# Kernel optimization log

Measured on AMD Instinct MI355X. Metric: run time of the kernel, lower is better.

## Reference

```python
import jax, jax.numpy as jnp
import numpy as np

V, BLK, L, H, C, FF = 50257, 2048, 6, 8, 512, 2048
D = C // H  # head_dim = 64

def setup_inputs() -> dict:
    key = jax.random.key(0)
    ks = jax.random.split(key, 16)
    s = 0.02
    proj_std = 0.02 / np.sqrt(2 * L)
    return {
        'idx': jax.random.randint(ks[0], (2, 2048), 0, V, dtype=jnp.int64),
        'wte': jax.random.normal(ks[1], (V, C), jnp.float32) * s,
        'wpe': jax.random.normal(ks[2], (BLK, C), jnp.float32) * s,
        'ln1_w': jnp.ones((L, C), jnp.float32), 'ln1_b': jnp.zeros((L, C), jnp.float32),
        'c_attn_w': jax.random.normal(ks[3], (L, 3 * C, C), jnp.float32) * s,
        'c_proj_w': jax.random.normal(ks[4], (L, C, C), jnp.float32) * proj_std,
        'ln2_w': jnp.ones((L, C), jnp.float32), 'ln2_b': jnp.zeros((L, C), jnp.float32),
        'fc_w': jax.random.normal(ks[5], (L, FF, C), jnp.float32) * s,
        'proj_w': jax.random.normal(ks[6], (L, C, FF), jnp.float32) * proj_std,
        'lnf_w': jnp.ones((C,), jnp.float32), 'lnf_b': jnp.zeros((C,), jnp.float32),
    }

def _layernorm(x, w, b, eps=1e-5):
    mu = jnp.mean(x, axis=-1, keepdims=True)
    var = jnp.var(x, axis=-1, keepdims=True)
    return (x - mu) * jax.lax.rsqrt(var + eps) * w + b

def _attn(x, attn_w, proj_w, mask):
    B, T, _ = x.shape
    qkv = jnp.einsum('btc,fc->btf', x, attn_w)  # (B,T,3C)
    q, k, v = jnp.split(qkv, 3, axis=-1)
    q = q.reshape(B, T, H, D)
    k = k.reshape(B, T, H, D)
    v = v.reshape(B, T, H, D)
    scale = 1.0 / np.sqrt(D)
    att = jnp.einsum('bthd,bshd->bhts', q, k) * scale  # (B,H,T,T)
    att = jnp.where(mask, att, -jnp.inf)
    att = jax.nn.softmax(att, axis=-1)
    y = jnp.einsum('bhts,bshd->bthd', att, v).reshape(B, T, C)
    return jnp.einsum('btc,oc->bto', y, proj_w)

def reference(idx, wte, wpe, ln1_w, ln1_b, c_attn_w, c_proj_w, ln2_w, ln2_b, fc_w, proj_w, lnf_w, lnf_b):
    B, T = idx.shape
    pos = jnp.arange(T)
    x = wte[idx] + wpe[pos]  # (B,T,C); dropout p=0
    mask = jnp.tril(jnp.ones((T, T), bool))[None, None]
    for i in range(L):
        x = x + _attn(_layernorm(x, ln1_w[i], ln1_b[i]), c_attn_w[i], c_proj_w[i], mask)
        h = _layernorm(x, ln2_w[i], ln2_b[i])
        h = jax.nn.gelu(jnp.einsum('btc,fc->btf', h, fc_w[i]), approximate=False)
        x = x + jnp.einsum('btf,cf->btc', h, proj_w[i])
    x = _layernorm(x, lnf_w, lnf_b)
    logits = jnp.einsum('btc,vc->btv', x, wte)  # tied lm_head
    return logits
```

## Files before the change

kernel.cpp:

```cpp
#include <hip/hip_runtime.h>

typedef unsigned short u16;
typedef short bf16x8 __attribute__((ext_vector_type(8)));
typedef float f32x4 __attribute__((ext_vector_type(4)));
typedef unsigned short u16x4 __attribute__((ext_vector_type(4)));
typedef unsigned short u16x8 __attribute__((ext_vector_type(8)));
typedef unsigned int u32x2 __attribute__((ext_vector_type(2)));

#define B_ 2
#define T_ 2048
#define C_ 512
#define H_ 8
#define FF_ 2048
#define L_ 6
#define V_ 50257
#define M_ (B_*T_)

__device__ __forceinline__ u16 f2b(float f) {
  union { float f; unsigned u; } v; v.f = f;
  unsigned r = v.u + 0x7FFFu + ((v.u >> 16) & 1u);
  return (u16)(r >> 16);
}
__device__ __forceinline__ float b2f(u16 u) {
  union { unsigned u; float f; } v; v.u = ((unsigned)u) << 16; return v.f;
}
__device__ __forceinline__ unsigned pk_bf16(float lo, float hi) {
  unsigned r;
  asm volatile("v_cvt_pk_bf16_f32 %0, %1, %2" : "=v"(r) : "v"(lo), "v"(hi));
  return r;
}
__device__ __forceinline__ float exp2_fast(float x) {
  float r; asm("v_exp_f32 %0, %1" : "=v"(r) : "v"(x)); return r;
}
__device__ __forceinline__ float rcp_fast(float x) {
  float r; asm("v_rcp_f32 %0, %1" : "=v"(r) : "v"(x)); return r;
}

__device__ __forceinline__ void async16(const void* g, void* l) {
  __builtin_amdgcn_global_load_lds((const __attribute__((address_space(1))) unsigned int*)g,
                                   (__attribute__((address_space(3))) unsigned int*)l, 16, 0, 0);
}

template<int N> __device__ __forceinline__ void vwait() {
  if constexpr (N == 0) asm volatile("s_waitcnt vmcnt(0)" ::: "memory");
  else if constexpr (N == 2) asm volatile("s_waitcnt vmcnt(2)" ::: "memory");
  else if constexpr (N == 3) asm volatile("s_waitcnt vmcnt(3)" ::: "memory");
  else if constexpr (N == 4) asm volatile("s_waitcnt vmcnt(4)" ::: "memory");
}

__device__ __forceinline__ bf16x8 scale8(u16x8 v, float s) {
  union { bf16x8 b; unsigned u[4]; } r;
#pragma unroll
  for (int i = 0; i < 4; i++)
    r.u[i] = pk_bf16(b2f(v[2*i]) * s, b2f(v[2*i+1]) * s);
  return r.b;
}

struct CvtArgs { const f32x4* s[5]; u16x4* d[5]; };
__global__ void cvt_all_k(CvtArgs a) {
  const int sizes[5] = { V_*C_/4, L_*3*C_*C_/4, L_*C_*C_/4, L_*FF_*C_/4, L_*C_*FF_/4 };
  int gid = blockIdx.x * blockDim.x + threadIdx.x;
  int stride = gridDim.x * blockDim.x;
#pragma unroll
  for (int seg = 0; seg < 5; seg++) {
    const f32x4* src = a.s[seg];
    u16x4* dst = a.d[seg];
    for (int i = gid; i < sizes[seg]; i += stride) {
      f32x4 v = src[i];
      u16x4 o;
      o[0] = f2b(v[0]); o[1] = f2b(v[1]); o[2] = f2b(v[2]); o[3] = f2b(v[3]);
      dst[i] = o;
    }
  }
}

__global__ void embed_k(const int* __restrict__ idx, const float* __restrict__ wte,
                        const float* __restrict__ wpe, float* __restrict__ x) {
  int t = blockIdx.x * 256 + threadIdx.x;
  int row = t >> 7;
  int c4 = t & 127;
  int tok = idx[row];
  int pos = row & (T_ - 1);
  f32x4 a = ((const f32x4*)(wte + (long)tok * C_))[c4];
  f32x4 p = ((const f32x4*)(wpe + (long)pos * C_))[c4];
  ((f32x4*)x)[t] = a + p;
}

__global__ void ln_k(const float* __restrict__ x, const float* __restrict__ w,
                     const float* __restrict__ b, u16* __restrict__ out) {
  int wv = threadIdx.x >> 6;
  int lane = threadIdx.x & 63;
  int row = blockIdx.x * 4 + wv;
  const f32x4* xr = (const f32x4*)(x + (long)row * C_);
  f32x4 v0 = xr[lane * 2], v1 = xr[lane * 2 + 1];
  float s = 0.f, s2 = 0.f;
#pragma unroll
  for (int j = 0; j < 4; j++) { s += v0[j] + v1[j]; s2 += v0[j]*v0[j] + v1[j]*v1[j]; }
#pragma unroll
  for (int off = 32; off >= 1; off >>= 1) { s += __shfl_xor(s, off); s2 += __shfl_xor(s2, off); }
  float mu = s * (1.f / C_);
  float inv = rsqrtf(s2 * (1.f / C_) - mu * mu + 1e-5f);
  const f32x4* wr = (const f32x4*)w;
  const f32x4* br = (const f32x4*)b;
  f32x4 w0 = wr[lane*2], w1 = wr[lane*2+1], b0 = br[lane*2], b1 = br[lane*2+1];
  u16x8 o;
#pragma unroll
  for (int j = 0; j < 4; j++) {
    o[j]     = f2b((v0[j] - mu) * inv * w0[j] + b0[j]);
    o[j + 4] = f2b((v1[j] - mu) * inv * w1[j] + b1[j]);
  }
  *(u16x8*)(out + (long)row * C_ + lane * 8) = o;
}

template<int EPI, int BM, int BN>
__global__ __launch_bounds__(256) void gemm_bt_k(
    const u16* __restrict__ A, const u16* __restrict__ Bw,
    u16* __restrict__ Cb, float* __restrict__ Cf,
    int N, int K, int ldc)
{
  constexpr int MT = BM / 32;
  constexpr int NT = BN / 32;
  constexpr int AJ = BM / 64;
  constexpr int BJ = BN / 64;
  constexpr int LPT = AJ + BJ;
  __shared__ __align__(16) u16 sA[3][BM * 32];
  __shared__ __align__(16) u16 sB[3][BN * 32];
  const int tid = threadIdx.x;
  const int n0 = blockIdx.x * BN;
  const int m0 = blockIdx.y * BM;
  const int w = tid >> 6;
  const int lane = tid & 63;
  const int wm = (w >> 1) * (BM / 2);
  const int wn = (w & 1) * (BN / 2);
  const int g = lane >> 4;
  const int l15 = lane & 15;
  const int sw3 = l15 & 3;

  f32x4 acc[MT][NT] = {};

  const int nk = K >> 5;
  const int ksw = ((tid & 3) ^ ((tid >> 2) & 3)) * 8;
  const u16* gA[AJ];
  const u16* gB[BJ];
#pragma unroll
  for (int j = 0; j < AJ; j++)
    gA[j] = A + (long)(m0 + (tid >> 2) + j * 64) * K + ksw;
#pragma unroll
  for (int j = 0; j < BJ; j++)
    gB[j] = Bw + (long)(n0 + (tid >> 2) + j * 64) * K + ksw;

  auto stage = [&](int buf, int kt) {
    int ko = kt << 5;
#pragma unroll
    for (int j = 0; j < AJ; j++)
      async16(gA[j] + ko, &sA[buf][(j * 256 + w * 64) * 8]);
#pragma unroll
    for (int j = 0; j < BJ; j++)
      async16(gB[j] + ko, &sB[buf][(j * 256 + w * 64) * 8]);
  };

  stage(0, 0);
  stage(1, 1);
  int cur = 0, nxt = 2;
  for (int kt = 0; kt < nk; kt++) {
    if (kt + 1 < nk) vwait<LPT>(); else vwait<0>();
    __builtin_amdgcn_s_barrier();
    if (kt + 2 < nk) stage(nxt, kt + 2);
    const u16* pa = sA[cur];
    const u16* pb = sB[cur];
    bf16x8 af[MT], bfr[NT];
#pragma unroll
    for (int mt = 0; mt < MT; mt++)
      af[mt] = *(const bf16x8*)(pa + (wm + mt * 16 + l15) * 32 + ((g ^ sw3) * 8));
#pragma unroll
    for (int nt = 0; nt < NT; nt++)
      bfr[nt] = *(const bf16x8*)(pb + (wn + nt * 16 + l15) * 32 + ((g ^ sw3) * 8));
#pragma unroll
    for (int mt = 0; mt < MT; mt++)
#pragma unroll
      for (int nt = 0; nt < NT; nt++)
        acc[mt][nt] = __builtin_amdgcn_mfma_f32_16x16x32_bf16(af[mt], bfr[nt], acc[mt][nt], 0, 0, 0);
    cur = (cur == 2) ? 0 : cur + 1;
    nxt = (nxt == 2) ? 0 : nxt + 1;
  }

#pragma unroll
  for (int mt = 0; mt < MT; mt++) {
    int m = m0 + wm + mt * 16 + g * 4;
#pragma unroll
    for (int nt = 0; nt < NT; nt++) {
      int n = n0 + wn + nt * 16 + l15;
      f32x4 v = acc[mt][nt];
#pragma unroll
      for (int r = 0; r < 4; r++) {
        long ci = (long)(m + r) * ldc + n;
        if (EPI == 0) {
          Cb[ci] = f2b(v[r]);
        } else if (EPI == 1) {
          Cf[ci] += v[r];
        } else {
          float f = v[r];
          float u = f * f;
          float inner = f * (0.7978845608028654f + 0.03567740814183056f * u);
          inner = fminf(fmaxf(inner, -15.f), 15.f);
          float a = exp2_fast(2.8853900817779268f * inner);
          Cb[ci] = f2b(f * a * rcp_fast(a + 1.0f));
        }
      }
    }
  }
}

__global__ __launch_bounds__(512) void gemm_lmhead_k(
    const u16* __restrict__ A, const u16* __restrict__ Bw,
    float* __restrict__ Cf, int N)
{
  __shared__ __align__(16) u16 sA[3][256 * 32];
  __shared__ __align__(16) u16 sB[3][128 * 32];
  const int K = 512;
  const int bid = blockIdx.x;
  const int swz = (bid & 7) * 786 + (bid >> 3);
  const int n0 = (swz % 393) * 128;
  const int m0 = (swz / 393) * 256;
  const int tid = threadIdx.x;
  const int w = tid >> 6;
  const int lane = tid & 63;
  const int wm = (w >> 1) * 64;
  const int wn = (w & 1) * 64;
  const int g = lane >> 4;
  const int l15 = lane & 15;
  const int sw3 = l15 & 3;

  f32x4 acc[4][4] = {};

  const int ksw = ((tid & 3) ^ ((tid >> 2) & 3)) * 8;
  const u16* gA[2];
#pragma unroll
  for (int j = 0; j < 2; j++)
    gA[j] = A + (long)(m0 + (tid >> 2) + j * 128) * K + ksw;
  int brow = n0 + (tid >> 2); if (brow > N - 1) brow = N - 1;
  const u16* gB0 = Bw + (long)brow * K + ksw;

  auto stage = [&](int buf, int kt) {
    int ko = kt << 5;
#pragma unroll
    for (int j = 0; j < 2; j++)
      async16(gA[j] + ko, &sA[buf][(j * 512 + w * 64) * 8]);
    async16(gB0 + ko, &sB[buf][(w * 64) * 8]);
  };

  stage(0, 0);
  stage(1, 1);
  int cur = 0, nxt = 2;
  const int nk = K >> 5;
  for (int kt = 0; kt < nk; kt++) {
    if (kt + 1 < nk) vwait<3>(); else vwait<0>();
    __builtin_amdgcn_s_barrier();
    if (kt + 2 < nk) stage(nxt, kt + 2);
    const u16* pa = sA[cur];
    const u16* pb = sB[cur];
    bf16x8 af[4], bfr[4];
#pragma unroll
    for (int mt = 0; mt < 4; mt++)
      af[mt] = *(const bf16x8*)(pa + (wm + mt * 16 + l15) * 32 + ((g ^ sw3) * 8));
#pragma unroll
    for (int nt = 0; nt < 4; nt++)
      bfr[nt] = *(const bf16x8*)(pb + (wn + nt * 16 + l15) * 32 + ((g ^ sw3) * 8));
#pragma unroll
    for (int mt = 0; mt < 4; mt++)
#pragma unroll
      for (int nt = 0; nt < 4; nt++)
        acc[mt][nt] = __builtin_amdgcn_mfma_f32_16x16x32_bf16(af[mt], bfr[nt], acc[mt][nt], 0, 0, 0);
    cur = (cur == 2) ? 0 : cur + 1;
    nxt = (nxt == 2) ? 0 : nxt + 1;
  }

#pragma unroll
  for (int mt = 0; mt < 4; mt++) {
    int m = m0 + wm + mt * 16 + g * 4;
#pragma unroll
    for (int nt = 0; nt < 4; nt++) {
      int n = n0 + wn + nt * 16 + l15;
      f32x4 v = acc[mt][nt];
      if (n < N) {
#pragma unroll
        for (int r = 0; r < 4; r++)
          Cf[(long)(m + r) * N + n] = v[r];
      }
    }
  }
}

__global__ __launch_bounds__(256) void attn_k(const u16* __restrict__ qkv, u16* __restrict__ out) {
  const int bh = blockIdx.y;
  const int b = bh >> 3;
  const int h = bh & 7;
  const int tid = threadIdx.x;
  const int wv = tid >> 6;
  const int lane = tid & 63;
  const int g = lane >> 4;
  const int l15 = lane & 15;
  const int qblk = 31 - blockIdx.x;

  __shared__ __align__(16) u16 Ks[2][64 * 64];
  __shared__ __align__(16) u16 Vt[2][64 * 72];
  __shared__ __align__(16) u16 Ps[4][16 * 64];

  const long base = (long)b * T_ * 1536;
  const u16* kbase = qkv + base + 512 + h * 64;
  const u16* vbase = qkv + base + 1024 + h * 64;
  const int kq = tid & 15;
  const int dg = (tid >> 4) & 7;
  const float qscale = 0.18033688011112042f;

  const int q0 = qblk * 64 + wv * 16;

  const u16* qrow = qkv + base + (long)(q0 + l15) * 1536 + h * 64;
  bf16x8 qf0 = scale8(*(const u16x8*)(qrow + g * 8), qscale);
  bf16x8 qf1 = scale8(*(const u16x8*)(qrow + 32 + g * 8), qscale);

  f32x4 o[4] = {};
  float mrun[4] = {-1e30f, -1e30f, -1e30f, -1e30f};
  float lrun[4] = {0.f, 0.f, 0.f, 0.f};
  const int kvend = qblk * 64 + 64;

  u16x8 vreg[4];
#pragma unroll
  for (int i = 0; i < 2; i++) {
    int chunk = i * 256 + tid;
    int row = chunk >> 3, c8 = chunk & 7;
    async16(kbase + (long)row * 1536 + (c8 ^ (row & 7)) * 8,
            &Ks[0][(i * 256 + wv * 64) * 8]);
  }
  if (tid < 128) {
#pragma unroll
    for (int t = 0; t < 4; t++)
      vreg[t] = *(const u16x8*)(vbase + (long)(kq + 16 * t) * 1536 + dg * 8);
#pragma unroll
    for (int e = 0; e < 8; e++) {
      int d = dg * 8 + e;
      u32x2 wq = { (unsigned)vreg[0][e] | ((unsigned)vreg[1][e] << 16),
                   (unsigned)vreg[2][e] | ((unsigned)vreg[3][e] << 16) };
      *(u32x2*)(&Vt[0][d * 72 + kq * 4]) = wq;
    }
  }
  __syncthreads();

  int cur = 0;
  for (int j0 = 0; j0 < kvend; j0 += 64, cur ^= 1) {
    const bool more = (j0 + 64) < kvend;
    if (more) {
      int jn = j0 + 64;
#pragma unroll
      for (int i = 0; i < 2; i++) {
        int chunk = i * 256 + tid;
        int row = chunk >> 3, c8 = chunk & 7;
        async16(kbase + (long)(jn + row) * 1536 + (c8 ^ (row & 7)) * 8,
                &Ks[cur ^ 1][(i * 256 + wv * 64) * 8]);
      }
      if (tid < 128) {
#pragma unroll
        for (int t = 0; t < 4; t++)
          vreg[t] = *(const u16x8*)(vbase + (long)(jn + kq + 16 * t) * 1536 + dg * 8);
      }
    }

    f32x4 s[4] = {};
    const u16* kp = Ks[cur];
#pragma unroll
    for (int t = 0; t < 4; t++) {
      int row = t * 16 + l15;
      const u16* kr = kp + row * 64;
      bf16x8 k0 = *(const bf16x8*)(kr + ((g ^ (row & 7)) * 8));
      bf16x8 k1 = *(const bf16x8*)(kr + (((4 + g) ^ (row & 7)) * 8));
      s[t] = __builtin_amdgcn_mfma_f32_16x16x32_bf16(qf0, k0, s[t], 0, 0, 0);
      s[t] = __builtin_amdgcn_mfma_f32_16x16x32_bf16(qf1, k1, s[t], 0, 0, 0);
    }

    const bool diag = (j0 + 64) == kvend;
    u16* pw = Ps[wv];
#pragma unroll
    for (int r = 0; r < 4; r++) {
      int row = q0 + g * 4 + r;
      float v0 = s[0][r], v1 = s[1][r], v2 = s[2][r], v3 = s[3][r];
      if (diag) {
        if (j0 +      l15 > row) v0 = -1e30f;
        if (j0 + 16 + l15 > row) v1 = -1e30f;
        if (j0 + 32 + l15 > row) v2 = -1e30f;
        if (j0 + 48 + l15 > row) v3 = -1e30f;
      }
      float mloc = fmaxf(fmaxf(v0, v1), fmaxf(v2, v3));
      float m = mrun[r];
      if (!__all(mloc <= m + 8.0f)) {
        float mx = mloc;
        mx = fmaxf(mx, __shfl_xor(mx, 1));
        mx = fmaxf(mx, __shfl_xor(mx, 2));
        mx = fmaxf(mx, __shfl_xor(mx, 4));
        mx = fmaxf(mx, __shfl_xor(mx, 8));
        float mn = fmaxf(m, mx);
        float sc2 = exp2_fast(m - mn);
        lrun[r] *= sc2;
#pragma unroll
        for (int dt = 0; dt < 4; dt++) o[dt][r] *= sc2;
        m = mn; mrun[r] = mn;
      }
      float e0 = exp2_fast(v0 - m), e1 = exp2_fast(v1 - m);
      float e2 = exp2_fast(v2 - m), e3 = exp2_fast(v3 - m);
      lrun[r] += (e0 + e1) + (e2 + e3);
      u32x2 pkq = { pk_bf16(e0, e1), pk_bf16(e2, e3) };
      int prow = g * 4 + r;
      int byt = prow * 128 + ((((l15 >> 1) ^ (prow & 7)) << 4)) + (l15 & 1) * 8;
      *(u32x2*)((char*)pw + byt) = pkq;
    }

    const u16* vt = Vt[cur];
    bf16x8 pf0 = *(const bf16x8*)((char*)pw + l15 * 128 + (((g) ^ (l15 & 7)) << 4));
    bf16x8 pf1 = *(const bf16x8*)((char*)pw + l15 * 128 + (((4 + g) ^ (l15 & 7)) << 4));
#pragma unroll
    for (int dt = 0; dt < 4; dt++) {
      int d = dt * 16 + l15;
      bf16x8 vf0 = *(const bf16x8*)(vt + d * 72 + g * 8);
      bf16x8 vf1 = *(const bf16x8*)(vt + d * 72 + 32 + g * 8);
      o[dt] = __builtin_amdgcn_mfma_f32_16x16x32_bf16(pf0, vf0, o[dt], 0, 0, 0);
      o[dt] = __builtin_amdgcn_mfma_f32_16x16x32_bf16(pf1, vf1, o[dt], 0, 0, 0);
    }

    if (more && tid < 128) {
#pragma unroll
      for (int e = 0; e < 8; e++) {
        int d = dg * 8 + e;
        u32x2 wq = { (unsigned)vreg[0][e] | ((unsigned)vreg[1][e] << 16),
                     (unsigned)vreg[2][e] | ((unsigned)vreg[3][e] << 16) };
        *(u32x2*)(&Vt[cur ^ 1][d * 72 + kq * 4]) = wq;
      }
    }
    __syncthreads();
  }

#pragma unroll
  for (int r = 0; r < 4; r++) {
    float ls = lrun[r];
    ls += __shfl_xor(ls, 1); ls += __shfl_xor(ls, 2);
    ls += __shfl_xor(ls, 4); ls += __shfl_xor(ls, 8);
    float inv = 1.0f / ls;
    int row = q0 + g * 4 + r;
    u16* orow = out + (long)(b * T_ + row) * C_ + h * 64;
#pragma unroll
    for (int dt = 0; dt < 4; dt++)
      orow[dt * 16 + l15] = f2b(o[dt][r] * inv);
  }
}

extern "C" void kernel_launch(void* const* d_in, const int* in_sizes, int n_in,
                              void* d_out, int out_size, void* d_ws, size_t ws_size,
                              hipStream_t stream) {
  const int*   idx    = (const int*)  d_in[0];
  const float* wte    = (const float*)d_in[1];
  const float* wpe    = (const float*)d_in[2];
  const float* ln1w   = (const float*)d_in[3];
  const float* ln1b   = (const float*)d_in[4];
  const float* wattn  = (const float*)d_in[5];
  const float* wcproj = (const float*)d_in[6];
  const float* ln2w   = (const float*)d_in[7];
  const float* ln2b   = (const float*)d_in[8];
  const float* wfc    = (const float*)d_in[9];
  const float* wproj2 = (const float*)d_in[10];
  const float* lnfw   = (const float*)d_in[11];
  const float* lnfb   = (const float*)d_in[12];
  float* out = (float*)d_out;

  char* p = (char*)d_ws;
  size_t off = 0;
  auto alloc = [&](size_t bytes) -> void* {
    void* r = p + off; off += (bytes + 255) & ~(size_t)255; return r;
  };
  float* x    = (float*)alloc((size_t)M_ * C_ * 4);
  u16* xn     = (u16*)alloc((size_t)M_ * C_ * 2);
  u16* qkvb   = (u16*)alloc((size_t)M_ * 3 * C_ * 2);
  u16* attb   = (u16*)alloc((size_t)M_ * C_ * 2);
  u16* hb     = (u16*)alloc((size_t)M_ * FF_ * 2);
  u16* wteB   = (u16*)alloc((size_t)V_ * C_ * 2);
  u16* wattnB = (u16*)alloc((size_t)L_ * 3 * C_ * C_ * 2);
  u16* wprojB = (u16*)alloc((size_t)L_ * C_ * C_ * 2);
  u16* wfcB   = (u16*)alloc((size_t)L_ * FF_ * C_ * 2);
  u16* wp2B   = (u16*)alloc((size_t)L_ * C_ * FF_ * 2);
  if (off > ws_size) return;

  CvtArgs ca;
  ca.s[0] = (const f32x4*)wte;    ca.d[0] = (u16x4*)wteB;
  ca.s[1] = (const f32x4*)wattn;  ca.d[1] = (u16x4*)wattnB;
  ca.s[2] = (const f32x4*)wcproj; ca.d[2] = (u16x4*)wprojB;
  ca.s[3] = (const f32x4*)wfc;    ca.d[3] = (u16x4*)wfcB;
  ca.s[4] = (const f32x4*)wproj2; ca.d[4] = (u16x4*)wp2B;
  cvt_all_k<<<dim3(2048), dim3(256), 0, stream>>>(ca);

  embed_k<<<dim3(M_ * C_ / 4 / 256), dim3(256), 0, stream>>>(idx, wte, wpe, x);

  for (int l = 0; l < L_; l++) {
    ln_k<<<dim3(M_ / 4), dim3(256), 0, stream>>>(x, ln1w + l * C_, ln1b + l * C_, xn);
    gemm_bt_k<0, 64, 128><<<dim3(12, 64), dim3(256), 0, stream>>>(
        xn, wattnB + (size_t)l * 3 * C_ * C_, qkvb, nullptr, 3 * C_, C_, 3 * C_);
    attn_k<<<dim3(32, B_ * H_), dim3(256), 0, stream>>>(qkvb, attb);
    gemm_bt_k<1, 64, 64><<<dim3(8, 64), dim3(256), 0, stream>>>(
        attb, wprojB + (size_t)l * C_ * C_, nullptr, x, C_, C_, C_);
    ln_k<<<dim3(M_ / 4), dim3(256), 0, stream>>>(x, ln2w + l * C_, ln2b + l * C_, xn);
    gemm_bt_k<2, 128, 128><<<dim3(16, 32), dim3(256), 0, stream>>>(
        xn, wfcB + (size_t)l * FF_ * C_, hb, nullptr, FF_, C_, FF_);
    gemm_bt_k<1, 64, 64><<<dim3(8, 64), dim3(256), 0, stream>>>(
        hb, wp2B + (size_t)l * C_ * FF_, nullptr, x, C_, FF_, C_);
  }
  ln_k<<<dim3(M_ / 4), dim3(256), 0, stream>>>(x, lnfw, lnfb, xn);
  gemm_lmhead_k<<<dim3(8 * 786), dim3(512), 0, stream>>>(xn, wteB, out, V_);
}
```

Before: 1.297 ms.

## Enlarge lm-head tile to 256x256 and add BK=64 kernel for residual GEMMs

The LM-head GEMM tile grows from 256x128 to 256x256, with each wave computing 64x128. This halves the number of A-tile reloads and raises arithmetic intensity. It also wraps the MFMA loop in s_setprio to favour compute waves. The two residual-add GEMMs (attention proj and MLP proj) move to a new dedicated kernel with a 64-wide K step, which halves the number of barrier iterations. The trade-off is more accumulator registers in the LM head, which may lower occupancy, and a wave grid that is now coarser.

```diff
diff --git a/kernel.cpp b/kernel.cpp
--- a/kernel.cpp
+++ b/kernel.cpp
@@ -196,8 +196,6 @@
         long ci = (long)(m + r) * ldc + n;
         if (EPI == 0) {
           Cb[ci] = f2b(v[r]);
-        } else if (EPI == 1) {
-          Cf[ci] += v[r];
         } else {
           float f = v[r];
           float u = f * f;
@@ -211,42 +209,129 @@
   }
 }
 
+__global__ __launch_bounds__(256) void gemm_bt64_k(
+    const u16* __restrict__ A, const u16* __restrict__ Bw,
+    float* __restrict__ Cf, int N, int K, int ldc)
+{
+  __shared__ __align__(16) u16 sA[3][64 * 64];
+  __shared__ __align__(16) u16 sB[3][64 * 64];
+  const int tid = threadIdx.x;
+  const int n0 = blockIdx.x * 64;
+  const int m0 = blockIdx.y * 64;
+  const int w = tid >> 6;
+  const int lane = tid & 63;
+  const int wm = (w >> 1) * 32;
+  const int wn = (w & 1) * 32;
+  const int g = lane >> 4;
+  const int l15 = lane & 15;
+  const int sw3 = l15 & 3;
+
+  f32x4 acc[2][2] = {};
+
+  const int nk = K >> 6;
+  const int srow = tid >> 3;
+  const int sl = tid & 7;
+  const int kcol = (((sl & 4) | ((sl & 3) ^ (srow & 3)))) * 8;
+  const u16* gA[2];
+  const u16* gB[2];
+#pragma unroll
+  for (int j = 0; j < 2; j++) {
+    gA[j] = A + (long)(m0 + srow + j * 32) * K + kcol;
+    gB[j] = Bw + (long)(n0 + srow + j * 32) * K + kcol;
+  }
+
+  auto stage = [&](int buf, int kt) {
+    int ko = kt << 6;
+#pragma unroll
+    for (int j = 0; j < 2; j++)
+      async16(gA[j] + ko, &sA[buf][(j * 256 + w * 64) * 8]);
+#pragma unroll
+    for (int j = 0; j < 2; j++)
+      async16(gB[j] + ko, &sB[buf][(j * 256 + w * 64) * 8]);
+  };
+
+  stage(0, 0);
+  stage(1, 1);
+  int cur = 0, nxt = 2;
+  for (int kt = 0; kt < nk; kt++) {
+    if (kt + 1 < nk) vwait<4>(); else vwait<0>();
+    __builtin_amdgcn_s_barrier();
+    if (kt + 2 < nk) stage(nxt, kt + 2);
+    const u16* pa = sA[cur];
+    const u16* pb = sB[cur];
+#pragma unroll
+    for (int h = 0; h < 2; h++) {
+      bf16x8 af[2], bfr[2];
+#pragma unroll
+      for (int mt = 0; mt < 2; mt++)
+        af[mt] = *(const bf16x8*)(pa + (wm + mt * 16 + l15) * 64 + (((g ^ sw3) + h * 4) * 8));
+#pragma unroll
+      for (int nt = 0; nt < 2; nt++)
+        bfr[nt] = *(const bf16x8*)(pb + (wn + nt * 16 + l15) * 64 + (((g ^ sw3) + h * 4) * 8));
+#pragma unroll
+      for (int mt = 0; mt < 2; mt++)
+#pragma unroll
+        for (int nt = 0; nt < 2; nt++)
+          acc[mt][nt] = __builtin_amdgcn_mfma_f32_16x16x32_bf16(af[mt], bfr[nt], acc[mt][nt], 0, 0, 0);
+    }
+    cur = (cur == 2) ? 0 : cur + 1;
+    nxt = (nxt == 2) ? 0 : nxt + 1;
+  }
+
+#pragma unroll
+  for (int mt = 0; mt < 2; mt++) {
+    int m = m0 + wm + mt * 16 + g * 4;
+#pragma unroll
+    for (int nt = 0; nt < 2; nt++) {
+      int n = n0 + wn + nt * 16 + l15;
+      f32x4 v = acc[mt][nt];
+#pragma unroll
+      for (int r = 0; r < 4; r++)
+        Cf[(long)(m + r) * ldc + n] += v[r];
+    }
+  }
+}
+
 __global__ __launch_bounds__(512) void gemm_lmhead_k(
     const u16* __restrict__ A, const u16* __restrict__ Bw,
     float* __restrict__ Cf, int N)
 {
   __shared__ __align__(16) u16 sA[3][256 * 32];
-  __shared__ __align__(16) u16 sB[3][128 * 32];
+  __shared__ __align__(16) u16 sB[3][256 * 32];
   const int K = 512;
   const int bid = blockIdx.x;
-  const int swz = (bid & 7) * 786 + (bid >> 3);
-  const int n0 = (swz % 393) * 128;
-  const int m0 = (swz / 393) * 256;
+  const int swz = (bid & 7) * 394 + (bid >> 3);
+  const int m0 = (swz / 197) * 256;
+  const int n0 = (swz % 197) * 256;
   const int tid = threadIdx.x;
   const int w = tid >> 6;
   const int lane = tid & 63;
   const int wm = (w >> 1) * 64;
-  const int wn = (w & 1) * 64;
+  const int wn = (w & 1) * 128;
   const int g = lane >> 4;
   const int l15 = lane & 15;
   const int sw3 = l15 & 3;
 
-  f32x4 acc[4][4] = {};
+  f32x4 acc[4][8] = {};
 
   const int ksw = ((tid & 3) ^ ((tid >> 2) & 3)) * 8;
   const u16* gA[2];
-#pragma unroll
-  for (int j = 0; j < 2; j++)
+  const u16* gB[2];
+#pragma unroll
+  for (int j = 0; j < 2; j++) {
     gA[j] = A + (long)(m0 + (tid >> 2) + j * 128) * K + ksw;
-  int brow = n0 + (tid >> 2); if (brow > N - 1) brow = N - 1;
-  const u16* gB0 = Bw + (long)brow * K + ksw;
+    int brow = n0 + (tid >> 2) + j * 128; if (brow > N - 1) brow = N - 1;
+    gB[j] = Bw + (long)brow * K + ksw;
+  }
 
   auto stage = [&](int buf, int kt) {
     int ko = kt << 5;
 #pragma unroll
     for (int j = 0; j < 2; j++)
       async16(gA[j] + ko, &sA[buf][(j * 512 + w * 64) * 8]);
-    async16(gB0 + ko, &sB[buf][(w * 64) * 8]);
+#pragma unroll
+    for (int j = 0; j < 2; j++)
+      async16(gB[j] + ko, &sB[buf][(j * 512 + w * 64) * 8]);
   };
 
   stage(0, 0);
@@ -254,23 +339,25 @@
   int cur = 0, nxt = 2;
   const int nk = K >> 5;
   for (int kt = 0; kt < nk; kt++) {
-    if (kt + 1 < nk) vwait<3>(); else vwait<0>();
+    if (kt + 1 < nk) vwait<4>(); else vwait<0>();
     __builtin_amdgcn_s_barrier();
     if (kt + 2 < nk) stage(nxt, kt + 2);
     const u16* pa = sA[cur];
     const u16* pb = sB[cur];
-    bf16x8 af[4], bfr[4];
+    bf16x8 af[4], bfr[8];
 #pragma unroll
     for (int mt = 0; mt < 4; mt++)
       af[mt] = *(const bf16x8*)(pa + (wm + mt * 16 + l15) * 32 + ((g ^ sw3) * 8));
 #pragma unroll
-    for (int nt = 0; nt < 4; nt++)
+    for (int nt = 0; nt < 8; nt++)
       bfr[nt] = *(const bf16x8*)(pb + (wn + nt * 16 + l15) * 32 + ((g ^ sw3) * 8));
+    __builtin_amdgcn_s_setprio(1);
 #pragma unroll
     for (int mt = 0; mt < 4; mt++)
 #pragma unroll
-      for (int nt = 0; nt < 4; nt++)
+      for (int nt = 0; nt < 8; nt++)
         acc[mt][nt] = __builtin_amdgcn_mfma_f32_16x16x32_bf16(af[mt], bfr[nt], acc[mt][nt], 0, 0, 0);
+    __builtin_amdgcn_s_setprio(0);
     cur = (cur == 2) ? 0 : cur + 1;
     nxt = (nxt == 2) ? 0 : nxt + 1;
   }
@@ -279,7 +366,7 @@
   for (int mt = 0; mt < 4; mt++) {
     int m = m0 + wm + mt * 16 + g * 4;
 #pragma unroll
-    for (int nt = 0; nt < 4; nt++) {
+    for (int nt = 0; nt < 8; nt++) {
       int n = n0 + wn + nt * 16 + l15;
       f32x4 v = acc[mt][nt];
       if (n < N) {
@@ -501,14 +588,14 @@
     gemm_bt_k<0, 64, 128><<<dim3(12, 64), dim3(256), 0, stream>>>(
         xn, wattnB + (size_t)l * 3 * C_ * C_, qkvb, nullptr, 3 * C_, C_, 3 * C_);
     attn_k<<<dim3(32, B_ * H_), dim3(256), 0, stream>>>(qkvb, attb);
-    gemm_bt_k<1, 64, 64><<<dim3(8, 64), dim3(256), 0, stream>>>(
-        attb, wprojB + (size_t)l * C_ * C_, nullptr, x, C_, C_, C_);
+    gemm_bt64_k<<<dim3(8, 64), dim3(256), 0, stream>>>(
+        attb, wprojB + (size_t)l * C_ * C_, x, C_, C_, C_);
     ln_k<<<dim3(M_ / 4), dim3(256), 0, stream>>>(x, ln2w + l * C_, ln2b + l * C_, xn);
     gemm_bt_k<2, 128, 128><<<dim3(16, 32), dim3(256), 0, stream>>>(
         xn, wfcB + (size_t)l * FF_ * C_, hb, nullptr, FF_, C_, FF_);
-    gemm_bt_k<1, 64, 64><<<dim3(8, 64), dim3(256), 0, stream>>>(
-        hb, wp2B + (size_t)l * C_ * FF_, nullptr, x, C_, FF_, C_);
+    gemm_bt64_k<<<dim3(8, 64), dim3(256), 0, stream>>>(
+        hb, wp2B + (size_t)l * C_ * FF_, x, C_, FF_, C_);
   }
   ln_k<<<dim3(M_ / 4), dim3(256), 0, stream>>>(x, lnfw, lnfb, xn);
-  gemm_lmhead_k<<<dim3(8 * 786), dim3(512), 0, stream>>>(xn, wteB, out, V_);
-}
+  gemm_lmhead_k<<<dim3(16 * 197), dim3(512), 0, stream>>>(xn, wteB, out, V_);
+}
```

Result: faster. 1.258 ms (-3.0%).

## Deepen GEMM K-step to 64 and enlarge lm-head tile to 256x256

Applied to the files above, without the earlier changes.

The general GEMM now stages 64-wide K slices per pipeline step with a new swizzle, halving barrier and wait overhead per unit of work. The lm-head GEMM uses 256x256 tiles with 8 N-fragments per wave, raises wave priority around the MFMA block, and writes logits with nontemporal stores. The FC GEMM is retiled to 128x64. Costs are more LDS use and register pressure, which may reduce occupancy.

```diff
diff --git a/kernel.cpp b/kernel.cpp
--- a/kernel.cpp
+++ b/kernel.cpp
@@ -54,6 +54,14 @@
   for (int i = 0; i < 4; i++)
     r.u[i] = pk_bf16(b2f(v[2*i]) * s, b2f(v[2*i+1]) * s);
   return r.b;
+}
+
+__device__ __forceinline__ float gelu_f(float f) {
+  float u = f * f;
+  float inner = f * (0.7978845608028654f + 0.03567740814183056f * u);
+  inner = fminf(fmaxf(inner, -15.f), 15.f);
+  float a = exp2_fast(2.8853900817779268f * inner);
+  return f * a * rcp_fast(a + 1.0f);
 }
 
 struct CvtArgs { const f32x4* s[5]; u16x4* d[5]; };
@@ -113,18 +121,18 @@
 }
 
 template<int EPI, int BM, int BN>
-__global__ __launch_bounds__(256) void gemm_bt_k(
+__global__ __launch_bounds__(256) void gemm64_k(
     const u16* __restrict__ A, const u16* __restrict__ Bw,
     u16* __restrict__ Cb, float* __restrict__ Cf,
     int N, int K, int ldc)
 {
   constexpr int MT = BM / 32;
   constexpr int NT = BN / 32;
-  constexpr int AJ = BM / 64;
-  constexpr int BJ = BN / 64;
+  constexpr int AJ = BM / 32;
+  constexpr int BJ = BN / 32;
   constexpr int LPT = AJ + BJ;
-  __shared__ __align__(16) u16 sA[3][BM * 32];
-  __shared__ __align__(16) u16 sB[3][BN * 32];
+  __shared__ __align__(16) u16 sA[3][BM * 64];
+  __shared__ __align__(16) u16 sB[3][BN * 64];
   const int tid = threadIdx.x;
   const int n0 = blockIdx.x * BN;
   const int m0 = blockIdx.y * BM;
@@ -138,19 +146,21 @@
 
   f32x4 acc[MT][NT] = {};
 
-  const int nk = K >> 5;
-  const int ksw = ((tid & 3) ^ ((tid >> 2) & 3)) * 8;
+  const int nk = K >> 6;
+  const int srow = tid >> 3;
+  const int sl = tid & 7;
+  const int kcol = (((sl & 4) | ((sl & 3) ^ (srow & 3)))) * 8;
   const u16* gA[AJ];
   const u16* gB[BJ];
 #pragma unroll
   for (int j = 0; j < AJ; j++)
-    gA[j] = A + (long)(m0 + (tid >> 2) + j * 64) * K + ksw;
+    gA[j] = A + (long)(m0 + srow + j * 32) * K + kcol;
 #pragma unroll
   for (int j = 0; j < BJ; j++)
-    gB[j] = Bw + (long)(n0 + (tid >> 2) + j * 64) * K + ksw;
+    gB[j] = Bw + (long)(n0 + srow + j * 32) * K + kcol;
 
   auto stage = [&](int buf, int kt) {
-    int ko = kt << 5;
+    int ko = kt << 6;
 #pragma unroll
     for (int j = 0; j < AJ; j++)
       async16(gA[j] + ko, &sA[buf][(j * 256 + w * 64) * 8]);
@@ -168,18 +178,21 @@
     if (kt + 2 < nk) stage(nxt, kt + 2);
     const u16* pa = sA[cur];
     const u16* pb = sB[cur];
-    bf16x8 af[MT], bfr[NT];
-#pragma unroll
-    for (int mt = 0; mt < MT; mt++)
-      af[mt] = *(const bf16x8*)(pa + (wm + mt * 16 + l15) * 32 + ((g ^ sw3) * 8));
-#pragma unroll
-    for (int nt = 0; nt < NT; nt++)
-      bfr[nt] = *(const bf16x8*)(pb + (wn + nt * 16 + l15) * 32 + ((g ^ sw3) * 8));
-#pragma unroll
-    for (int mt = 0; mt < MT; mt++)
+#pragma unroll
+    for (int h = 0; h < 2; h++) {
+      bf16x8 af[MT], bfr[NT];
+#pragma unroll
+      for (int mt = 0; mt < MT; mt++)
+        af[mt] = *(const bf16x8*)(pa + (wm + mt * 16 + l15) * 64 + (((g ^ sw3) + h * 4) * 8));
 #pragma unroll
       for (int nt = 0; nt < NT; nt++)
-        acc[mt][nt] = __builtin_amdgcn_mfma_f32_16x16x32_bf16(af[mt], bfr[nt], acc[mt][nt], 0, 0, 0);
+        bfr[nt] = *(const bf16x8*)(pb + (wn + nt * 16 + l15) * 64 + (((g ^ sw3) + h * 4) * 8));
+#pragma unroll
+      for (int mt = 0; mt < MT; mt++)
+#pragma unroll
+        for (int nt = 0; nt < NT; nt++)
+          acc[mt][nt] = __builtin_amdgcn_mfma_f32_16x16x32_bf16(af[mt], bfr[nt], acc[mt][nt], 0, 0, 0);
+    }
     cur = (cur == 2) ? 0 : cur + 1;
     nxt = (nxt == 2) ? 0 : nxt + 1;
   }
@@ -199,12 +212,7 @@
         } else if (EPI == 1) {
           Cf[ci] += v[r];
         } else {
-          float f = v[r];
-          float u = f * f;
-          float inner = f * (0.7978845608028654f + 0.03567740814183056f * u);
-          inner = fminf(fmaxf(inner, -15.f), 15.f);
-          float a = exp2_fast(2.8853900817779268f * inner);
-          Cb[ci] = f2b(f * a * rcp_fast(a + 1.0f));
+          Cb[ci] = f2b(gelu_f(v[r]));
         }
       }
     }
@@ -216,37 +224,41 @@
     float* __restrict__ Cf, int N)
 {
   __shared__ __align__(16) u16 sA[3][256 * 32];
-  __shared__ __align__(16) u16 sB[3][128 * 32];
+  __shared__ __align__(16) u16 sB[3][256 * 32];
   const int K = 512;
   const int bid = blockIdx.x;
-  const int swz = (bid & 7) * 786 + (bid >> 3);
-  const int n0 = (swz % 393) * 128;
-  const int m0 = (swz / 393) * 256;
+  const int swz = (bid & 7) * 394 + (bid >> 3);
+  const int m0 = (swz / 197) * 256;
+  const int n0 = (swz % 197) * 256;
   const int tid = threadIdx.x;
   const int w = tid >> 6;
   const int lane = tid & 63;
   const int wm = (w >> 1) * 64;
-  const int wn = (w & 1) * 64;
+  const int wn = (w & 1) * 128;
   const int g = lane >> 4;
   const int l15 = lane & 15;
   const int sw3 = l15 & 3;
 
-  f32x4 acc[4][4] = {};
+  f32x4 acc[4][8] = {};
 
   const int ksw = ((tid & 3) ^ ((tid >> 2) & 3)) * 8;
   const u16* gA[2];
-#pragma unroll
-  for (int j = 0; j < 2; j++)
+  const u16* gB[2];
+#pragma unroll
+  for (int j = 0; j < 2; j++) {
     gA[j] = A + (long)(m0 + (tid >> 2) + j * 128) * K + ksw;
-  int brow = n0 + (tid >> 2); if (brow > N - 1) brow = N - 1;
-  const u16* gB0 = Bw + (long)brow * K + ksw;
+    int brow = n0 + (tid >> 2) + j * 128; if (brow > N - 1) brow = N - 1;
+    gB[j] = Bw + (long)brow * K + ksw;
+  }
 
   auto stage = [&](int buf, int kt) {
     int ko = kt << 5;
 #pragma unroll
     for (int j = 0; j < 2; j++)
       async16(gA[j] + ko, &sA[buf][(j * 512 + w * 64) * 8]);
-    async16(gB0 + ko, &sB[buf][(w * 64) * 8]);
+#pragma unroll
+    for (int j = 0; j < 2; j++)
+      async16(gB[j] + ko, &sB[buf][(j * 512 + w * 64) * 8]);
   };
 
   stage(0, 0);
@@ -254,23 +266,25 @@
   int cur = 0, nxt = 2;
   const int nk = K >> 5;
   for (int kt = 0; kt < nk; kt++) {
-    if (kt + 1 < nk) vwait<3>(); else vwait<0>();
+    if (kt + 1 < nk) vwait<4>(); else vwait<0>();
     __builtin_amdgcn_s_barrier();
     if (kt + 2 < nk) stage(nxt, kt + 2);
     const u16* pa = sA[cur];
     const u16* pb = sB[cur];
-    bf16x8 af[4], bfr[4];
+    bf16x8 af[4], bfr[8];
 #pragma unroll
     for (int mt = 0; mt < 4; mt++)
       af[mt] = *(const bf16x8*)(pa + (wm + mt * 16 + l15) * 32 + ((g ^ sw3) * 8));
 #pragma unroll
-    for (int nt = 0; nt < 4; nt++)
+    for (int nt = 0; nt < 8; nt++)
       bfr[nt] = *(const bf16x8*)(pb + (wn + nt * 16 + l15) * 32 + ((g ^ sw3) * 8));
+    __builtin_amdgcn_s_setprio(1);
 #pragma unroll
     for (int mt = 0; mt < 4; mt++)
 #pragma unroll
-      for (int nt = 0; nt < 4; nt++)
+      for (int nt = 0; nt < 8; nt++)
         acc[mt][nt] = __builtin_amdgcn_mfma_f32_16x16x32_bf16(af[mt], bfr[nt], acc[mt][nt], 0, 0, 0);
+    __builtin_amdgcn_s_setprio(0);
     cur = (cur == 2) ? 0 : cur + 1;
     nxt = (nxt == 2) ? 0 : nxt + 1;
   }
@@ -279,13 +293,13 @@
   for (int mt = 0; mt < 4; mt++) {
     int m = m0 + wm + mt * 16 + g * 4;
 #pragma unroll
-    for (int nt = 0; nt < 4; nt++) {
+    for (int nt = 0; nt < 8; nt++) {
       int n = n0 + wn + nt * 16 + l15;
       f32x4 v = acc[mt][nt];
       if (n < N) {
 #pragma unroll
         for (int r = 0; r < 4; r++)
-          Cf[(long)(m + r) * N + n] = v[r];
+          __builtin_nontemporal_store(v[r], &Cf[(long)(m + r) * N + n]);
       }
     }
   }
@@ -498,17 +512,17 @@
 
   for (int l = 0; l < L_; l++) {
     ln_k<<<dim3(M_ / 4), dim3(256), 0, stream>>>(x, ln1w + l * C_, ln1b + l * C_, xn);
-    gemm_bt_k<0, 64, 128><<<dim3(12, 64), dim3(256), 0, stream>>>(
+    gemm64_k<0, 64, 128><<<dim3(12, 64), dim3(256), 0, stream>>>(
         xn, wattnB + (size_t)l * 3 * C_ * C_, qkvb, nullptr, 3 * C_, C_, 3 * C_);
     attn_k<<<dim3(32, B_ * H_), dim3(256), 0, stream>>>(qkvb, attb);
-    gemm_bt_k<1, 64, 64><<<dim3(8, 64), dim3(256), 0, stream>>>(
+    gemm64_k<1, 64, 64><<<dim3(8, 64), dim3(256), 0, stream>>>(
         attb, wprojB + (size_t)l * C_ * C_, nullptr, x, C_, C_, C_);
     ln_k<<<dim3(M_ / 4), dim3(256), 0, stream>>>(x, ln2w + l * C_, ln2b + l * C_, xn);
-    gemm_bt_k<2, 128, 128><<<dim3(16, 32), dim3(256), 0, stream>>>(
+    gemm64_k<2, 128, 64><<<dim3(32, 32), dim3(256), 0, stream>>>(
         xn, wfcB + (size_t)l * FF_ * C_, hb, nullptr, FF_, C_, FF_);
-    gemm_bt_k<1, 64, 64><<<dim3(8, 64), dim3(256), 0, stream>>>(
+    gemm64_k<1, 64, 64><<<dim3(8, 64), dim3(256), 0, stream>>>(
         hb, wp2B + (size_t)l * C_ * FF_, nullptr, x, C_, FF_, C_);
   }
   ln_k<<<dim3(M_ / 4), dim3(256), 0, stream>>>(x, lnfw, lnfb, xn);
-  gemm_lmhead_k<<<dim3(8 * 786), dim3(512), 0, stream>>>(xn, wteB, out, V_);
-}
+  gemm_lmhead_k<<<dim3(16 * 197), dim3(512), 0, stream>>>(xn, wteB, out, V_);
+}
```

Result: slower. 1.624 ms (+25.2%).
